# Performance work log

Hardware: AMD Instinct MI355X
Metric: run time of the kernel (lower is better)

Reference implementation:

```python
import jax, jax.numpy as jnp
import numpy as np

B, N, E, D, H, HW, L = 16, 32, 256, 256, 8, 784, 4
DH = D // H
FF = 4 * D
BN = B * N
BE = B * E
SCALE = 1.0 / np.sqrt(DH)


def _ln(x, g, b):
    m = x.mean(-1, keepdims=True)
    v = ((x - m) ** 2).mean(-1, keepdims=True)
    return (x - m) * jax.lax.rsqrt(v + 1e-5) * g + b


def setup_inputs() -> dict:
    key = jax.random.key(0)
    ks = iter(jax.random.split(key, 64))
    def w(shape, s=0.05):
        return jax.random.normal(next(ks), shape, jnp.float32) * s
    inp = {
        'nodes': w((B, N, D), 1.0),
        'edges': w((B, E, D), 1.0),
        'images': w((B, HW, D), 1.0),
        'mask': jnp.zeros((B * H, N + E, HW), jnp.float32),
        'node_enc': w((BN, D), 1.0),
        'edge_enc': w((BE, D), 1.0),
        'ln1_g': jnp.ones((L, D), jnp.float32), 'ln1_b': jnp.zeros((L, D), jnp.float32),
        'Wqkv': w((L, D, 3 * D)), 'bqkv': jnp.zeros((L, 3 * D), jnp.float32),
        'Wo': w((L, D, D)), 'bo': jnp.zeros((L, D), jnp.float32),
        'ls1': jnp.full((L, D), 0.1, jnp.float32),
        'ln2_g': jnp.ones((L, D), jnp.float32), 'ln2_b': jnp.zeros((L, D), jnp.float32),
        'Wn1': w((L, D, D)), 'bn1': jnp.zeros((L, D), jnp.float32),
        'Wn2': w((L, D, D)), 'bn2': jnp.zeros((L, D), jnp.float32),
        'We': w((L, D, D)), 'be': jnp.zeros((L, D), jnp.float32),
        'attn_p': w((L, H, DH), 1.0),
        'Weo': w((L, D, D)), 'beo': jnp.zeros((L, D), jnp.float32),
        'Wno': w((L, D, D)), 'bno': jnp.zeros((L, D), jnp.float32),
        'ls2': jnp.full((L, D), 0.1, jnp.float32),
        'ln3_g': jnp.ones((L, D), jnp.float32), 'ln3_b': jnp.zeros((L, D), jnp.float32),
        'W1': w((L, D, FF)), 'b1': jnp.zeros((L, FF), jnp.float32),
        'W2': w((L, FF, D)), 'b2': jnp.zeros((L, D), jnp.float32),
        'ls3': jnp.full((L, D), 0.1, jnp.float32),
        'edge_index': jax.random.randint(next(ks), (2, BE), 0, BN, jnp.int32),
    }
    return inp


def reference(nodes, edges, images, mask, node_enc, edge_enc,
              ln1_g, ln1_b, Wqkv, bqkv, Wo, bo, ls1,
              ln2_g, ln2_b, Wn1, bn1, Wn2, bn2, We, be, attn_p, Weo, beo, Wno, bno, ls2,
              ln3_g, ln3_b, W1, b1, W2, b2, ls3, edge_index):
    idx0, idx1 = edge_index[0], edge_index[1]
    ne = jnp.concatenate([nodes, edges], axis=1)  # [B, N+E, D]
    mask4 = mask.reshape(B, H, N + E, HW)
    for l in range(L):
        # cross-attention ne -> images
        ne1n = _ln(ne, ln1_g[l], ln1_b[l])
        q = (ne1n @ Wqkv[l, :, :D] + bqkv[l, :D]).reshape(B, N + E, H, DH)
        k = (images @ Wqkv[l, :, D:2 * D] + bqkv[l, D:2 * D]).reshape(B, HW, H, DH)
        v = (images @ Wqkv[l, :, 2 * D:] + bqkv[l, 2 * D:]).reshape(B, HW, H, DH)
        scores = jnp.einsum('bqhd,bkhd->bhqk', q, k) * SCALE + mask4
        attn = jax.nn.softmax(scores, axis=-1)
        ctx = jnp.einsum('bhqk,bkhd->bqhd', attn, v).reshape(B, N + E, D)
        ne1 = ne + ls1[l] * (ctx @ Wo[l] + bo[l])
        # modified GAT on flattened graph
        ne2n = _ln(ne1, ln2_g[l], ln2_b[l])
        nodes_f = ne2n[:, :N].reshape(BN, D) + node_enc
        edges_f = ne2n[:, N:].reshape(BE, D) + edge_enc
        fn = (nodes_f @ Wn1[l] + bn1[l])[idx0]
        sn = (nodes_f @ Wn2[l] + bn2[l])[idx0]  # NOTE: original code uses edge_index[0] here too
        ep = edges_f @ We[l] + be[l]
        hidden = jax.nn.gelu(fn + sn + ep, approximate=False)  # [BE, D]
        pres = (hidden.reshape(BE, H, DH) * attn_p[l]).sum(-1)  # [BE, H]
        mseg = jax.ops.segment_max(pres, idx0, num_segments=BN)
        expv = jnp.exp(pres - mseg[idx0])
        denom = jax.ops.segment_sum(expv, idx0, num_segments=BN)
        alpha = expv / denom[idx0]  # scatter_softmax over destination nodes
        new_edges = hidden @ Weo[l] + beo[l]
        vals = (nodes_f[idx1] + new_edges) @ Wno[l] + bno[l]
        vals = vals.reshape(BE, H, DH) * alpha[..., None]
        new_nodes = jax.ops.segment_sum(vals.reshape(BE, D), idx0, num_segments=BN)
        gat = jnp.concatenate([new_nodes.reshape(B, N, D), new_edges.reshape(B, E, D)], axis=1)
        ne2 = ne1 + ls2[l] * gat
        # FFN
        ne3n = _ln(ne2, ln3_g[l], ln3_b[l])
        ffn = jax.nn.gelu(ne3n @ W1[l] + b1[l], approximate=False) @ W2[l] + b2[l]
        ne = ne2 + ls3[l] * ffn
    return ne
```

## Files before the change

kernel.cpp:

```cpp
#include <hip/hip_runtime.h>
#include <math.h>

static constexpr int B_  = 16;
static constexpr int N_  = 32;
static constexpr int E_  = 256;
static constexpr int D_  = 256;
static constexpr int H_  = 8;
static constexpr int HW_ = 784;
static constexpr int L_  = 4;
static constexpr int DH_ = 32;
static constexpr int FF_ = 1024;
static constexpr int BN_ = 512;
static constexpr int BE_ = 4096;
static constexpr int NE_ = 288;
static constexpr int NC_ = 13;
static constexpr int NBLK_ = B_ * H_ * 9;
#define SCALE_ 0.17677669529663687f

static constexpr size_t LAYER_W = 1114112;
static constexpr size_t OFF_Q   = 0;
static constexpr size_t OFF_K   = 65536;
static constexpr size_t OFF_WO  = 196608;
static constexpr size_t OFF_WN1 = 262144;
static constexpr size_t OFF_WE  = 393216;
static constexpr size_t OFF_WEO = 458752;
static constexpr size_t OFF_WNO = 524288;
static constexpr size_t OFF_W1  = 589824;
static constexpr size_t OFF_W2  = 851968;

typedef __attribute__((ext_vector_type(8))) short bf16x8;
typedef __attribute__((ext_vector_type(4))) float f32x4;

typedef __attribute__((address_space(1))) const unsigned int gas_uint;
typedef __attribute__((address_space(3))) unsigned int las_uint;

__device__ __forceinline__ void gload16(const unsigned short* g, unsigned short* lds) {
    __builtin_amdgcn_global_load_lds((gas_uint*)g, (las_uint*)lds, 16, 0, 0);
}

__device__ __forceinline__ float gelu_f(float x) {
    return 0.5f * x * (1.0f + erff(x * 0.7071067811865476f));
}

__device__ __forceinline__ unsigned short f2bf(float x) {
    unsigned u = __float_as_uint(x);
    u += 0x7FFFu + ((u >> 16) & 1u);
    return (unsigned short)(u >> 16);
}
__device__ __forceinline__ unsigned pack2bf(float a, float b) {
    return (unsigned)f2bf(a) | ((unsigned)f2bf(b) << 16);
}
__device__ __forceinline__ float bf2f(unsigned short u) {
    return __uint_as_float(((unsigned)u) << 16);
}


__global__ void concat_kernel(const float* __restrict__ nodes, const float* __restrict__ edges,
                              float* __restrict__ ne) {
    int tid = blockIdx.x * 256 + threadIdx.x;
    int d = tid & 255;
    int row = tid >> 8;
    int b = row / NE_, pos = row % NE_;
    float v = (pos < N_) ? nodes[(size_t)(b * N_ + pos) * D_ + d]
                         : edges[(size_t)(b * E_ + (pos - N_)) * D_ + d];
    ne[tid] = v;
}

__global__ void imgcast_kernel(const float* __restrict__ img, unsigned short* __restrict__ out) {
    int tid = blockIdx.x * 256 + threadIdx.x;
    const float* p = img + (size_t)tid * 8;
    float4 a = *(const float4*)(p);
    float4 b = *(const float4*)(p + 4);
    uint4 o = make_uint4(pack2bf(a.x, a.y), pack2bf(a.z, a.w),
                         pack2bf(b.x, b.y), pack2bf(b.z, b.w));
    *(uint4*)&out[(size_t)tid * 8] = o;
}

__global__ void zeroinit_kernel(int* counts, int* maskflag) {
    int t = blockIdx.x * 256 + threadIdx.x;
    if (t < BN_) counts[t] = 0;
    if (t == 0) *maskflag = 0;
}

__global__ __launch_bounds__(256) void maskchk_kernel(const float* __restrict__ mask,
                                                      int* __restrict__ flag) {
    const size_t total = (size_t)B_ * H_ * NE_ * HW_ / 4;
    const uint4* m = (const uint4*)mask;
    unsigned acc = 0;
    for (size_t i = (size_t)blockIdx.x * 256 + threadIdx.x; i < total; i += (size_t)gridDim.x * 256) {
        uint4 v = m[i];
        acc |= v.x | v.y | v.z | v.w;
    }
    unsigned long long bal = __ballot(acc != 0);
    if (bal != 0 && (threadIdx.x & 63) == (__ffsll((long long)bal) - 1))
        atomicOr(flag, 1);
}

__global__ __launch_bounds__(128) void premask_kernel(const float* __restrict__ mask,
                                                      unsigned short* __restrict__ pmask,
                                                      const int* __restrict__ flag) {
    if (*flag == 0) return;
    const int bid = blockIdx.x;
    const int c = bid % NC_;
    const int bq = bid / NC_;
    const int h = bq & 7;
    const int qt = (bq >> 3) % 9;
    const int b = (bq >> 3) / 9;
    const int q0 = qt * 32, c0 = c * 64;
    __shared__ float ts[32][68];
    const int t = threadIdx.x;
    const int row = t >> 2, cg = (t & 3) * 16;
    const float* mrow = mask + ((size_t)(b * H_ + h) * NE_ + q0 + row) * (size_t)HW_;
    #pragma unroll
    for (int i = 0; i < 4; ++i) {
        int col = c0 + cg + i * 4;
        float4 m4;
        if (col + 4 <= HW_) {
            m4 = *(const float4*)(mrow + col);
        } else {
            m4.x = (col + 0 < HW_) ? mrow[col + 0] : -1e30f;
            m4.y = (col + 1 < HW_) ? mrow[col + 1] : -1e30f;
            m4.z = (col + 2 < HW_) ? mrow[col + 2] : -1e30f;
            m4.w = (col + 3 < HW_) ? mrow[col + 3] : -1e30f;
        }
        *(float4*)&ts[row][cg + i * 4] = m4;
    }
    __syncthreads();
    const int w = t >> 6, lg = (t & 63) >> 4, lr = t & 15;
    const int r0 = w * 16 + lg * 4;
    unsigned u[8];
    #pragma unroll
    for (int rg = 0; rg < 4; ++rg) {
        u[rg * 2 + 0] = pack2bf(ts[r0 + rg][0 * 16 + lr], ts[r0 + rg][1 * 16 + lr]);
        u[rg * 2 + 1] = pack2bf(ts[r0 + rg][2 * 16 + lr], ts[r0 + rg][3 * 16 + lr]);
    }
    uint4* dst = (uint4*)(pmask + (size_t)bid * 2048 + t * 16);
    dst[0] = make_uint4(u[0], u[1], u[2], u[3]);
    dst[1] = make_uint4(u[4], u[5], u[6], u[7]);
}

__device__ __forceinline__ float ln_from_val(float v, int d,
                                             const float* __restrict__ g, const float* __restrict__ bta,
                                             float* sh1, float* sh2) {
    float s = v, s2 = v * v;
    #pragma unroll
    for (int o = 32; o >= 1; o >>= 1) { s += __shfl_down(s, o); s2 += __shfl_down(s2, o); }
    int lane = d & 63, w = d >> 6;
    if (lane == 0) { sh1[w] = s; sh2[w] = s2; }
    __syncthreads();
    if (d == 0) {
        float a = sh1[0] + sh1[1] + sh1[2] + sh1[3];
        float c = sh2[0] + sh2[1] + sh2[2] + sh2[3];
        sh1[0] = a; sh2[0] = c;
    }
    __syncthreads();
    float mean = sh1[0] * (1.0f / D_);
    float var  = sh2[0] * (1.0f / D_) - mean * mean;
    float rstd = rsqrtf(var + 1e-5f);
    return (v - mean) * rstd * g[d] + bta[d];
}

__global__ __launch_bounds__(256) void ln_kernel(const float* __restrict__ x,
                                                 unsigned short* __restrict__ y,
                                                 const float* __restrict__ g,
                                                 const float* __restrict__ bta) {
    __shared__ float sh1[4], sh2[4];
    const int row = blockIdx.x, d = threadIdx.x;
    float v = x[(size_t)row * D_ + d];
    y[(size_t)row * D_ + d] = f2bf(ln_from_val(v, d, g, bta, sh1, sh2));
}

__global__ __launch_bounds__(256) void ln2enc_kernel(const float* __restrict__ x,
                                                     const float* __restrict__ g,
                                                     const float* __restrict__ bta,
                                                     const float* __restrict__ node_enc,
                                                     const float* __restrict__ edge_enc,
                                                     unsigned short* __restrict__ nodes_f,
                                                     unsigned short* __restrict__ edges_f) {
    __shared__ float sh1[4], sh2[4];
    const int row = blockIdx.x, d = threadIdx.x;
    float v = x[(size_t)row * D_ + d];
    float val = ln_from_val(v, d, g, bta, sh1, sh2);
    int b = row / NE_, pos = row % NE_;
    if (pos < N_) {
        int rn = b * N_ + pos;
        nodes_f[(size_t)rn * D_ + d] = f2bf(val + node_enc[(size_t)rn * D_ + d]);
    } else {
        int re = b * E_ + (pos - N_);
        edges_f[(size_t)re * D_ + d] = f2bf(val + edge_enc[(size_t)re * D_ + d]);
    }
}

__global__ __launch_bounds__(256) void gatres_ln_kernel(
    float* __restrict__ ne, const float* __restrict__ new_nodes,
    const float* __restrict__ new_edges, const float* __restrict__ ls2l,
    const float* __restrict__ g, const float* __restrict__ bta,
    unsigned short* __restrict__ lnb) {
    __shared__ float sh1[4], sh2[4];
    const int row = blockIdx.x, d = threadIdx.x;
    int b = row / NE_, pos = row % NE_;
    float gv = (pos < N_) ? new_nodes[(size_t)(b * N_ + pos) * D_ + d]
                          : new_edges[(size_t)(b * E_ + (pos - N_)) * D_ + d];
    float v = ne[(size_t)row * D_ + d] + ls2l[d] * gv;
    ne[(size_t)row * D_ + d] = v;
    lnb[(size_t)row * D_ + d] = f2bf(ln_from_val(v, d, g, bta, sh1, sh2));
}

__global__ __launch_bounds__(256) void wtrans_kernel(
    const float* __restrict__ Wqkv, const float* __restrict__ Wo,
    const float* __restrict__ Wn1,  const float* __restrict__ Wn2,
    const float* __restrict__ We,   const float* __restrict__ Weo,
    const float* __restrict__ Wno,  const float* __restrict__ W1,
    const float* __restrict__ W2,   unsigned short* __restrict__ wT)
{
    const int bid = blockIdx.x;
    const int l = bid / 1088;
    int tl = bid % 1088;
    const float* src; int ld, K, Nn; unsigned short* dst;
    if (tl < 576) {
        int mid = tl >> 6; tl &= 63;
        K = 256; Nn = 256;
        if (mid < 3) {
            src = Wqkv + (size_t)l * 256 * 768 + mid * 256; ld = 768;
            dst = wT + (size_t)l * LAYER_W + (size_t)mid * 65536;
        } else {
            const float* bases[6] = {Wo, Wn1, Wn2, We, Weo, Wno};
            src = bases[mid - 3] + (size_t)l * 65536; ld = 256;
            dst = wT + (size_t)l * LAYER_W + OFF_WO + (size_t)(mid - 3) * 65536;
        }
    } else if (tl < 832) {
        tl -= 576; K = 256; Nn = 1024;
        src = W1 + (size_t)l * 262144; ld = 1024;
        dst = wT + (size_t)l * LAYER_W + OFF_W1;
    } else {
        tl -= 832; K = 1024; Nn = 256;
        src = W2 + (size_t)l * 262144; ld = 256;
        dst = wT + (size_t)l * LAYER_W + OFF_W2;
    }
    const int ntn = Nn >> 5;
    const int k0 = (tl / ntn) << 5, n0 = (tl % ntn) << 5;
    __shared__ float ts[32][33];
    const int t = threadIdx.x;
    const int kl = t >> 5, nl = t & 31;
    #pragma unroll
    for (int rr = 0; rr < 4; ++rr)
        ts[kl + rr * 8][nl] = src[(size_t)(k0 + kl + rr * 8) * ld + n0 + nl];
    __syncthreads();
    const int onl = t >> 3, okl = (t & 7) << 2;
    ushort4 o;
    o.x = f2bf(ts[okl + 0][onl]); o.y = f2bf(ts[okl + 1][onl]);
    o.z = f2bf(ts[okl + 2][onl]); o.w = f2bf(ts[okl + 3][onl]);
    *(ushort4*)&dst[(size_t)(n0 + onl) * K + k0 + okl] = o;
}


struct GArgs {
    const unsigned short* A;
    const unsigned short* Bt;
    const float* bias;
    const float* bias2;
    void* C;
    int lda, ldc, K, outbf, nbx;
};

template<int MODE, int OUTBF>
__global__ __launch_bounds__(256) void mgemm_kernel(
    const unsigned short* __restrict__ A, int lda,
    const unsigned short* __restrict__ Bt,
    const float* __restrict__ bias,
    const float* __restrict__ bias2,
    const float* __restrict__ res,
    const float* __restrict__ ls,
    void* __restrict__ Cv, int ldc, int K)
{
    __shared__ __align__(16) unsigned short As[64 * 64];
    __shared__ __align__(16) unsigned short Bs[64 * 64];
    const int m0 = blockIdx.y * 64, n0 = blockIdx.x * 64;
    const int t = threadIdx.x;
    const int l = t & 63, w = t >> 6;
    const int wr = (w >> 1) * 32, wc = (w & 1) * 32;
    const int frow = l & 15, kg = l >> 4;
    const int srow = w * 8 + (l >> 3);
    const int scolh = 8 * ((l & 7) ^ (l >> 3));
    const int ldsoff = w * 512;
    const int sw = (frow & 7) << 3;
    f32x4 acc[2][2];
    acc[0][0] = (f32x4){0.f,0.f,0.f,0.f}; acc[0][1] = acc[0][0];
    acc[1][0] = acc[0][0];                acc[1][1] = acc[0][0];
    for (int k0 = 0; k0 < K; k0 += 64) {
        const unsigned short* ga = A  + (size_t)(m0 + srow) * lda + k0 + scolh;
        const unsigned short* gb = Bt + (size_t)(n0 + srow) * K   + k0 + scolh;
        gload16(ga,                As + ldsoff);
        gload16(ga + 32 * lda,     As + ldsoff + 2048);
        gload16(gb,                Bs + ldsoff);
        gload16(gb + (size_t)32 * K, Bs + ldsoff + 2048);
        __syncthreads();
        #pragma unroll
        for (int kk = 0; kk < 2; ++kk) {
            const int off = (kk * 32 + kg * 8) ^ sw;
            bf16x8 af0 = *(const bf16x8*)&As[(wr + frow) * 64 + off];
            bf16x8 af1 = *(const bf16x8*)&As[(wr + 16 + frow) * 64 + off];
            bf16x8 bf0 = *(const bf16x8*)&Bs[(wc + frow) * 64 + off];
            bf16x8 bf1 = *(const bf16x8*)&Bs[(wc + 16 + frow) * 64 + off];
            acc[0][0] = __builtin_amdgcn_mfma_f32_16x16x32_bf16(af0, bf0, acc[0][0], 0, 0, 0);
            acc[0][1] = __builtin_amdgcn_mfma_f32_16x16x32_bf16(af0, bf1, acc[0][1], 0, 0, 0);
            acc[1][0] = __builtin_amdgcn_mfma_f32_16x16x32_bf16(af1, bf0, acc[1][0], 0, 0, 0);
            acc[1][1] = __builtin_amdgcn_mfma_f32_16x16x32_bf16(af1, bf1, acc[1][1], 0, 0, 0);
        }
        __syncthreads();
    }
    #pragma unroll
    for (int fr = 0; fr < 2; ++fr) {
        #pragma unroll
        for (int fc = 0; fc < 2; ++fc) {
            int n = n0 + wc + fc * 16 + frow;
            float bv = (bias2 != nullptr && n >= 256) ? bias2[n - 256] : bias[n];
            float lv = (MODE == 2) ? ls[n] : 0.f;
            #pragma unroll
            for (int rg = 0; rg < 4; ++rg) {
                int m = m0 + wr + fr * 16 + kg * 4 + rg;
                float vv = acc[fr][fc][rg] + bv;
                if (MODE == 1) vv = gelu_f(vv);
                if (MODE == 2) vv = res[(size_t)m * ldc + n] + lv * vv;
                if (OUTBF) ((unsigned short*)Cv)[(size_t)m * ldc + n] = f2bf(vv);
                else       ((float*)Cv)[(size_t)m * ldc + n] = vv;
            }
        }
    }
}

__global__ __launch_bounds__(256) void mgemm2_kernel(GArgs g0, GArgs g1, int nblk0) {
    const bool first = (int)blockIdx.x < nblk0;
    GArgs g = first ? g0 : g1;
    const int bid = first ? blockIdx.x : blockIdx.x - nblk0;
    __shared__ __align__(16) unsigned short As[64 * 64];
    __shared__ __align__(16) unsigned short Bs[64 * 64];
    const int m0 = (bid / g.nbx) * 64, n0 = (bid % g.nbx) * 64;
    const int t = threadIdx.x;
    const int l = t & 63, w = t >> 6;
    const int wr = (w >> 1) * 32, wc = (w & 1) * 32;
    const int frow = l & 15, kg = l >> 4;
    const int srow = w * 8 + (l >> 3);
    const int scolh = 8 * ((l & 7) ^ (l >> 3));
    const int ldsoff = w * 512;
    const int sw = (frow & 7) << 3;
    f32x4 acc[2][2];
    acc[0][0] = (f32x4){0.f,0.f,0.f,0.f}; acc[0][1] = acc[0][0];
    acc[1][0] = acc[0][0];                acc[1][1] = acc[0][0];
    for (int k0 = 0; k0 < g.K; k0 += 64) {
        const unsigned short* ga = g.A  + (size_t)(m0 + srow) * g.lda + k0 + scolh;
        const unsigned short* gb = g.Bt + (size_t)(n0 + srow) * g.K   + k0 + scolh;
        gload16(ga,                  As + ldsoff);
        gload16(ga + 32 * g.lda,     As + ldsoff + 2048);
        gload16(gb,                  Bs + ldsoff);
        gload16(gb + (size_t)32 * g.K, Bs + ldsoff + 2048);
        __syncthreads();
        #pragma unroll
        for (int kk = 0; kk < 2; ++kk) {
            const int off = (kk * 32 + kg * 8) ^ sw;
            bf16x8 af0 = *(const bf16x8*)&As[(wr + frow) * 64 + off];
            bf16x8 af1 = *(const bf16x8*)&As[(wr + 16 + frow) * 64 + off];
            bf16x8 bf0 = *(const bf16x8*)&Bs[(wc + frow) * 64 + off];
            bf16x8 bf1 = *(const bf16x8*)&Bs[(wc + 16 + frow) * 64 + off];
            acc[0][0] = __builtin_amdgcn_mfma_f32_16x16x32_bf16(af0, bf0, acc[0][0], 0, 0, 0);
            acc[0][1] = __builtin_amdgcn_mfma_f32_16x16x32_bf16(af0, bf1, acc[0][1], 0, 0, 0);
            acc[1][0] = __builtin_amdgcn_mfma_f32_16x16x32_bf16(af1, bf0, acc[1][0], 0, 0, 0);
            acc[1][1] = __builtin_amdgcn_mfma_f32_16x16x32_bf16(af1, bf1, acc[1][1], 0, 0, 0);
        }
        __syncthreads();
    }
    #pragma unroll
    for (int fr = 0; fr < 2; ++fr) {
        #pragma unroll
        for (int fc = 0; fc < 2; ++fc) {
            int n = n0 + wc + fc * 16 + frow;
            float bv = (g.bias2 != nullptr && n >= 256) ? g.bias2[n - 256] : g.bias[n];
            #pragma unroll
            for (int rg = 0; rg < 4; ++rg) {
                int m = m0 + wr + fr * 16 + kg * 4 + rg;
                float vv = acc[fr][fc][rg] + bv;
                if (g.outbf) ((unsigned short*)g.C)[(size_t)m * g.ldc + n] = f2bf(vv);
                else         ((float*)g.C)[(size_t)m * g.ldc + n] = vv;
            }
        }
    }
}

__global__ __launch_bounds__(128) void attn_kernel(
    const unsigned short* __restrict__ q, const unsigned short* __restrict__ kv,
    const unsigned short* __restrict__ pmask, const int* __restrict__ maskflag,
    unsigned short* __restrict__ ctx)
{
    const int bid = blockIdx.x;
    const int h = bid & 7;
    const int qt = (bid >> 3) % 9;
    const int b = (bid >> 3) / 9;
    const int q0 = qt * 32;
    const int t = threadIdx.x;
    const int w = t >> 6, l = t & 63;
    const int lr = l & 15, lg = l >> 4;
    const int hasmask = *maskflag;

    __shared__ unsigned short Ks[2][64][40];
    __shared__ unsigned short Vs[2][32][72];
    __shared__ unsigned short Pl[2][16][72];

    bf16x8 qfrag = *(const bf16x8*)(q + ((size_t)(b * NE_ + q0 + w * 16 + lr)) * D_ + h * DH_ + lg * 8);

    const int kkey = t >> 1, kdh = (t & 1) * 16;
    const int vdh = (t & 7) * 4, vk0 = (t >> 3) * 2;
    const unsigned short* kbase = kv + ((size_t)b * HW_) * 512 + h * DH_;
    const unsigned short* vbase = kv + ((size_t)b * HW_) * 512 + 256 + h * DH_;
    const uint4* mbase = (const uint4*)(pmask + (size_t)bid * NC_ * 2048 + t * 16);

    uint4 kq0, kq1;
    ushort4 va[2], vb4[2];
    uint4 mc0 = make_uint4(0,0,0,0), mc1 = mc0, mn0 = mc0, mn1 = mc0;

    auto issue_kv = [&](int c0) {
        {
            int key = c0 + kkey;
            bool ok = key < HW_;
            const unsigned short* kp = kbase + (size_t)(ok ? key : 0) * 512 + kdh;
            kq0 = *(const uint4*)(kp);
            kq1 = *(const uint4*)(kp + 8);
            if (!ok) { kq0 = make_uint4(0,0,0,0); kq1 = kq0; }
        }
        #pragma unroll
        for (int r = 0; r < 2; ++r) {
            int key = c0 + vk0 + 32 * r;
            bool ok0 = key < HW_, ok1 = (key + 1) < HW_;
            const unsigned short* vp = vbase + (size_t)(ok0 ? key : 0) * 512 + vdh;
            va[r]  = *(const ushort4*)(vp);
            vb4[r] = *(const ushort4*)(vp + (ok1 ? 512 : 0));
            if (!ok0) va[r]  = make_ushort4(0,0,0,0);
            if (!ok1) vb4[r] = make_ushort4(0,0,0,0);
        }
    };
    auto write_kv = [&](int bufi) {
        *(uint4*)&Ks[bufi][kkey][kdh]     = kq0;
        *(uint4*)&Ks[bufi][kkey][kdh + 8] = kq1;
        #pragma unroll
        for (int r = 0; r < 2; ++r) {
            const unsigned short* a = (const unsigned short*)&va[r];
            const unsigned short* c = (const unsigned short*)&vb4[r];
            #pragma unroll
            for (int i = 0; i < 4; ++i)
                *(unsigned*)&Vs[bufi][vdh + i][vk0 + 32 * r] = (unsigned)a[i] | ((unsigned)c[i] << 16);
        }
    };

    f32x4 oacc[2];
    oacc[0] = (f32x4){0.f, 0.f, 0.f, 0.f}; oacc[1] = oacc[0];
    float m_i[4] = {-INFINITY, -INFINITY, -INFINITY, -INFINITY};
    float l_i[4] = {0.f, 0.f, 0.f, 0.f};

    issue_kv(0);
    if (hasmask) { mc0 = mbase[0]; mc1 = mbase[1]; }
    write_kv(0);
    if (hasmask) { mn0 = mbase[128]; mn1 = mbase[129]; }
    __syncthreads();

    for (int c = 0; c < NC_; ++c) {
        const int c0 = c * 64;
        const int cb = c & 1, nb = cb ^ 1;
        if (c + 1 < NC_) issue_kv(c0 + 64);

        f32x4 sacc[4];
        #pragma unroll
        for (int fc = 0; fc < 4; ++fc) {
            sacc[fc] = (f32x4){0.f, 0.f, 0.f, 0.f};
            bf16x8 kf = *(const bf16x8*)&Ks[cb][fc * 16 + lr][lg * 8];
            sacc[fc] = __builtin_amdgcn_mfma_f32_16x16x32_bf16(qfrag, kf, sacc[fc], 0, 0, 0);
        }
        float s[4][4];
        if (hasmask) {
            unsigned uw[8] = {mc0.x, mc0.y, mc0.z, mc0.w, mc1.x, mc1.y, mc1.z, mc1.w};
            #pragma unroll
            for (int rg = 0; rg < 4; ++rg) {
                s[0][rg] = sacc[0][rg] * SCALE_ + bf2f((unsigned short)(uw[rg * 2] & 0xffff));
                s[1][rg] = sacc[1][rg] * SCALE_ + bf2f((unsigned short)(uw[rg * 2] >> 16));
                s[2][rg] = sacc[2][rg] * SCALE_ + bf2f((unsigned short)(uw[rg * 2 + 1] & 0xffff));
                s[3][rg] = sacc[3][rg] * SCALE_ + bf2f((unsigned short)(uw[rg * 2 + 1] >> 16));
            }
        } else {
            const bool tailc = (c == NC_ - 1);
            #pragma unroll
            for (int fc = 0; fc < 4; ++fc) {
                float pad = (tailc && (c0 + fc * 16 + lr) >= HW_) ? -1e30f : 0.f;
                #pragma unroll
                for (int rg = 0; rg < 4; ++rg)
                    s[fc][rg] = sacc[fc][rg] * SCALE_ + pad;
            }
        }

        float mloc[4];
        #pragma unroll
        for (int rg = 0; rg < 4; ++rg)
            mloc[rg] = fmaxf(fmaxf(s[0][rg], s[1][rg]), fmaxf(s[2][rg], s[3][rg]));
        #pragma unroll
        for (int off = 1; off < 16; off <<= 1)
            #pragma unroll
            for (int rg = 0; rg < 4; ++rg)
                mloc[rg] = fmaxf(mloc[rg], __shfl_xor(mloc[rg], off));
        float scl[4], lloc[4];
        #pragma unroll
        for (int rg = 0; rg < 4; ++rg) {
            float mn = fmaxf(m_i[rg], mloc[rg]);
            scl[rg] = __expf(m_i[rg] - mn);
            m_i[rg] = mn;
        }
        #pragma unroll
        for (int rg = 0; rg < 4; ++rg) {
            float acc = 0.f;
            #pragma unroll
            for (int fc = 0; fc < 4; ++fc) {
                float p = __expf(s[fc][rg] - m_i[rg]);
                s[fc][rg] = p;
                acc += p;
            }
            lloc[rg] = acc;
        }
        #pragma unroll
        for (int off = 1; off < 16; off <<= 1)
            #pragma unroll
            for (int rg = 0; rg < 4; ++rg)
                lloc[rg] += __shfl_xor(lloc[rg], off);
        #pragma unroll
        for (int rg = 0; rg < 4; ++rg) {
            l_i[rg] = l_i[rg] * scl[rg] + lloc[rg];
            oacc[0][rg] *= scl[rg];
            oacc[1][rg] *= scl[rg];
        }

        #pragma unroll
        for (int fc = 0; fc < 4; ++fc)
            #pragma unroll
            for (int rg = 0; rg < 4; ++rg)
                Pl[w][lg * 4 + rg][fc * 16 + lr] = f2bf(s[fc][rg]);
        #pragma unroll
        for (int ks2 = 0; ks2 < 2; ++ks2) {
            bf16x8 pf = *(const bf16x8*)&Pl[w][lr][ks2 * 32 + lg * 8];
            #pragma unroll
            for (int d2 = 0; d2 < 2; ++d2) {
                bf16x8 vf = *(const bf16x8*)&Vs[cb][d2 * 16 + lr][ks2 * 32 + lg * 8];
                oacc[d2] = __builtin_amdgcn_mfma_f32_16x16x32_bf16(pf, vf, oacc[d2], 0, 0, 0);
            }
        }

        if (hasmask) {
            mc0 = mn0; mc1 = mn1;
            if (c + 2 < NC_) {
                mn0 = mbase[(c + 2) * 128];
                mn1 = mbase[(c + 2) * 128 + 1];
            }
        }
        if (c + 1 < NC_) {
            write_kv(nb);
            __syncthreads();
        }
    }

    unsigned short* cbase = ctx + ((size_t)(b * NE_ + q0 + w * 16 + lg * 4)) * D_ + h * DH_;
    #pragma unroll
    for (int rg = 0; rg < 4; ++rg) {
        float inv = 1.0f / l_i[rg];
        #pragma unroll
        for (int d2 = 0; d2 < 2; ++d2)
            cbase[(size_t)rg * D_ + d2 * 16 + lr] = f2bf(oacc[d2][rg] * inv);
    }
}


__global__ __launch_bounds__(256) void hidden_kernel(
    const float* __restrict__ gn12,
    unsigned short* __restrict__ hid, const int* __restrict__ idx0,
    const float* __restrict__ attn_p_l, float* __restrict__ pres) {
    int e = blockIdx.x;
    int d = threadIdx.x;
    int n = idx0[e];
    float x = bf2f(hid[(size_t)e * D_ + d]) + gn12[(size_t)n * 512 + d] + gn12[(size_t)n * 512 + 256 + d];
    float hv = gelu_f(x);
    hid[(size_t)e * D_ + d] = f2bf(hv);
    float pr = hv * attn_p_l[d];
    #pragma unroll
    for (int o = 1; o < 32; o <<= 1) pr += __shfl_xor(pr, o);
    if ((d & 31) == 0) pres[e * H_ + (d >> 5)] = pr;
}

__global__ void segsoft_kernel(const float* __restrict__ pres, const int* __restrict__ csr_off,
                               const int* __restrict__ csr_perm,
                               float* __restrict__ mseg, float* __restrict__ denom) {
    int tid = blockIdx.x * 256 + threadIdx.x;
    int n = tid >> 3, h = tid & 7;
    int s = csr_off[n], e2 = csr_off[n + 1];
    float mx = -INFINITY;
    for (int i = s; i < e2; ++i) mx = fmaxf(mx, pres[csr_perm[i] * H_ + h]);
    float sum = 0.f;
    for (int i = s; i < e2; ++i) sum += expf(pres[csr_perm[i] * H_ + h] - mx);
    mseg[tid] = mx;
    denom[tid] = sum;
}

__global__ void vin_kernel(const unsigned short* __restrict__ nodes_f,
                           const float* __restrict__ new_edges,
                           const int* __restrict__ idx1, unsigned short* __restrict__ vin) {
    int tid = blockIdx.x * 256 + threadIdx.x;
    int e = tid >> 8, d = tid & 255;
    vin[tid] = f2bf(bf2f(nodes_f[(size_t)idx1[e] * D_ + d]) + new_edges[tid]);
}

__global__ __launch_bounds__(256) void nodeagg_kernel(
    const float* __restrict__ vals, const float* __restrict__ pres,
    const float* __restrict__ mseg, const float* __restrict__ denom,
    const int* __restrict__ csr_off, const int* __restrict__ csr_perm,
    float* __restrict__ new_nodes) {
    int n = blockIdx.x;
    int d = threadIdx.x;
    int s = csr_off[n], e2 = csr_off[n + 1];
    int h = d >> 5;
    float ms = mseg[n * H_ + h];
    float rd = 1.0f / denom[n * H_ + h];
    float acc = 0.f;
    for (int i = s; i < e2; ++i) {
        int e = csr_perm[i];
        float a = expf(pres[e * H_ + h] - ms) * rd;
        acc += vals[(size_t)e * D_ + d] * a;
    }
    new_nodes[(size_t)n * D_ + d] = acc;
}


__global__ void csr_count(const int* __restrict__ idx0, int* __restrict__ counts) {
    int e = blockIdx.x * 256 + threadIdx.x;
    if (e < BE_) atomicAdd(&counts[idx0[e]], 1);
}

__global__ __launch_bounds__(512) void csr_scan(const int* __restrict__ counts, int* __restrict__ csr_off) {
    __shared__ int buf[BN_];
    int t = threadIdx.x;
    int c = counts[t];
    buf[t] = c;
    __syncthreads();
    for (int o = 1; o < BN_; o <<= 1) {
        int add = (t >= o) ? buf[t - o] : 0;
        __syncthreads();
        buf[t] += add;
        __syncthreads();
    }
    csr_off[t] = buf[t] - c;
    if (t == BN_ - 1) csr_off[BN_] = buf[t];
}

__global__ __launch_bounds__(64) void csr_fill(const int* __restrict__ idx0,
                                               const int* __restrict__ csr_off,
                                               int* __restrict__ csr_perm) {
    int n = blockIdx.x;
    int lane = threadIdx.x;
    int w = csr_off[n];
    for (int c0 = 0; c0 < BE_; c0 += 64) {
        int e = c0 + lane;
        bool m = (idx0[e] == n);
        unsigned long long bal = __ballot(m);
        if (m) {
            int pre = __popcll(bal & ((1ull << lane) - 1ull));
            csr_perm[w + pre] = e;
        }
        w += __popcll(bal);
    }
}


static void launch_mgemm(hipStream_t s, int mode, int outbf,
                         const unsigned short* A, int lda, const unsigned short* Bt,
                         const float* bias, const float* bias2, const float* res, const float* ls,
                         void* C, int ldc, int M, int N, int K) {
    dim3 g(N / 64, M / 64);
    if (mode == 0) {
        if (outbf) mgemm_kernel<0,1><<<g, 256, 0, s>>>(A, lda, Bt, bias, bias2, res, ls, C, ldc, K);
        else       mgemm_kernel<0,0><<<g, 256, 0, s>>>(A, lda, Bt, bias, bias2, res, ls, C, ldc, K);
    } else if (mode == 1) {
        mgemm_kernel<1,1><<<g, 256, 0, s>>>(A, lda, Bt, bias, bias2, res, ls, C, ldc, K);
    } else {
        mgemm_kernel<2,0><<<g, 256, 0, s>>>(A, lda, Bt, bias, bias2, res, ls, C, ldc, K);
    }
}

extern "C" void kernel_launch(void* const* d_in, const int* in_sizes, int n_in,
                              void* d_out, int out_size, void* d_ws, size_t ws_size,
                              hipStream_t stream) {
    const float* nodes    = (const float*)d_in[0];
    const float* edges    = (const float*)d_in[1];
    const float* images   = (const float*)d_in[2];
    const float* mask     = (const float*)d_in[3];
    const float* node_enc = (const float*)d_in[4];
    const float* edge_enc = (const float*)d_in[5];
    const float* ln1_g = (const float*)d_in[6];
    const float* ln1_b = (const float*)d_in[7];
    const float* Wqkv  = (const float*)d_in[8];
    const float* bqkv  = (const float*)d_in[9];
    const float* Wo    = (const float*)d_in[10];
    const float* bo    = (const float*)d_in[11];
    const float* ls1   = (const float*)d_in[12];
    const float* ln2_g = (const float*)d_in[13];
    const float* ln2_b = (const float*)d_in[14];
    const float* Wn1   = (const float*)d_in[15];
    const float* bn1   = (const float*)d_in[16];
    const float* Wn2   = (const float*)d_in[17];
    const float* bn2   = (const float*)d_in[18];
    const float* We    = (const float*)d_in[19];
    const float* be    = (const float*)d_in[20];
    const float* attn_p= (const float*)d_in[21];
    const float* Weo   = (const float*)d_in[22];
    const float* beo   = (const float*)d_in[23];
    const float* Wno   = (const float*)d_in[24];
    const float* bno   = (const float*)d_in[25];
    const float* ls2   = (const float*)d_in[26];
    const float* ln3_g = (const float*)d_in[27];
    const float* ln3_b = (const float*)d_in[28];
    const float* W1    = (const float*)d_in[29];
    const float* b1    = (const float*)d_in[30];
    const float* W2    = (const float*)d_in[31];
    const float* b2    = (const float*)d_in[32];
    const float* ls3   = (const float*)d_in[33];
    const int*   edge_index = (const int*)d_in[34];
    const int* idx0 = edge_index;
    const int* idx1 = edge_index + BE_;

    float* ne = (float*)d_out;

    float* cur = (float*)d_ws;
    auto alloc = [&](size_t nfl) { float* p = cur; cur += nfl; return p; };
    auto allocbf = [&](size_t nbf) { float* p = cur; cur += (nbf + 1) / 2; return (unsigned short*)p; };

    unsigned short* lnbuf   = allocbf((size_t)B_ * NE_ * D_);
    unsigned short* qb      = allocbf((size_t)B_ * NE_ * D_);
    unsigned short* kvb     = allocbf((size_t)B_ * HW_ * 512);
    unsigned short* ffnh    = kvb;
    unsigned short* imgbf   = allocbf((size_t)B_ * HW_ * D_);
    unsigned short* ctxb    = allocbf((size_t)B_ * NE_ * D_);
    unsigned short* nodes_f = allocbf((size_t)BN_ * D_);
    unsigned short* edges_f = allocbf((size_t)BE_ * D_);
    unsigned short* hid     = allocbf((size_t)BE_ * D_);
    unsigned short* vin     = allocbf((size_t)BE_ * D_);
    unsigned short* pmaskb  = allocbf((size_t)NBLK_ * NC_ * 2048);
    float* gn12     = alloc((size_t)BN_ * 512);
    float* pres     = alloc((size_t)BE_ * H_);
    float* mseg     = alloc((size_t)BN_ * H_);
    float* denom    = alloc((size_t)BN_ * H_);
    float* new_edges= alloc((size_t)BE_ * D_);
    float* valsb    = alloc((size_t)BE_ * D_);
    float* new_nodes= alloc((size_t)BN_ * D_);
    int* counts   = (int*)cur; cur += BN_;
    int* csr_off  = (int*)cur; cur += BN_ + 4;
    int* csr_perm = (int*)cur; cur += BE_;
    int* maskflag = (int*)cur; cur += 4;
    cur = (float*)(((uintptr_t)cur + 255) & ~(uintptr_t)255);
    unsigned short* wT = (unsigned short*)cur;

    zeroinit_kernel<<<2, 256, 0, stream>>>(counts, maskflag);
    maskchk_kernel<<<2048, 256, 0, stream>>>(mask, maskflag);
    wtrans_kernel<<<4 * 1088, 256, 0, stream>>>(Wqkv, Wo, Wn1, Wn2, We, Weo, Wno, W1, W2, wT);
    imgcast_kernel<<<(B_ * HW_ * D_) / (256 * 8), 256, 0, stream>>>(images, imgbf);
    premask_kernel<<<NBLK_ * NC_, 128, 0, stream>>>(mask, pmaskb, maskflag);
    csr_count<<<BE_ / 256, 256, 0, stream>>>(idx0, counts);
    csr_scan<<<1, 512, 0, stream>>>(counts, csr_off);
    csr_fill<<<BN_, 64, 0, stream>>>(idx0, csr_off, csr_perm);
    concat_kernel<<<(B_ * NE_ * D_) / 256, 256, 0, stream>>>(nodes, edges, ne);

    for (int l = 0; l < L_; ++l) {
        const unsigned short* wTl = wT + (size_t)l * LAYER_W;
        const float* bqkv_l = bqkv + (size_t)l * 3 * D_;

        ln_kernel<<<B_ * NE_, 256, 0, stream>>>(ne, lnbuf, ln1_g + l * D_, ln1_b + l * D_);
        {
            GArgs gq { lnbuf, wTl + OFF_Q, bqkv_l, nullptr, qb, 256, 256, 256, 1, 4 };
            GArgs gkv{ imgbf, wTl + OFF_K, bqkv_l + D_, nullptr, kvb, 256, 512, 256, 1, 8 };
            int nb0 = (B_ * NE_ / 64) * 4;
            int nb1 = (B_ * HW_ / 64) * 8;
            mgemm2_kernel<<<nb0 + nb1, 256, 0, stream>>>(gq, gkv, nb0);
        }
        attn_kernel<<<NBLK_, 128, 0, stream>>>(qb, kvb, pmaskb, maskflag, ctxb);
        launch_mgemm(stream, 2, 0, ctxb, D_, wTl + OFF_WO, bo + l * D_, nullptr, ne, ls1 + l * D_,
                     ne, D_, B_ * NE_, D_, D_);

        ln2enc_kernel<<<B_ * NE_, 256, 0, stream>>>(ne, ln2_g + l * D_, ln2_b + l * D_,
                                                    node_enc, edge_enc, nodes_f, edges_f);
        {
            GArgs gn { nodes_f, wTl + OFF_WN1, bn1 + l * D_, bn2 + l * D_, gn12, 256, 512, 256, 0, 8 };
            GArgs ge { edges_f, wTl + OFF_WE,  be + l * D_,  nullptr,      hid,  256, 256, 256, 1, 4 };
            int nb0 = (BN_ / 64) * 8;
            int nb1 = (BE_ / 64) * 4;
            mgemm2_kernel<<<nb0 + nb1, 256, 0, stream>>>(gn, ge, nb0);
        }
        hidden_kernel<<<BE_, 256, 0, stream>>>(gn12, hid, idx0, attn_p + (size_t)l * H_ * DH_, pres);
        segsoft_kernel<<<(BN_ * H_) / 256, 256, 0, stream>>>(pres, csr_off, csr_perm, mseg, denom);
        launch_mgemm(stream, 0, 0, hid, D_, wTl + OFF_WEO, beo + l * D_, nullptr, nullptr, nullptr,
                     new_edges, D_, BE_, D_, D_);
        vin_kernel<<<(BE_ * D_) / 256, 256, 0, stream>>>(nodes_f, new_edges, idx1, vin);
        launch_mgemm(stream, 0, 0, vin, D_, wTl + OFF_WNO, bno + l * D_, nullptr, nullptr, nullptr,
                     valsb, D_, BE_, D_, D_);
        nodeagg_kernel<<<BN_, 256, 0, stream>>>(valsb, pres, mseg, denom, csr_off, csr_perm, new_nodes);
        gatres_ln_kernel<<<B_ * NE_, 256, 0, stream>>>(ne, new_nodes, new_edges, ls2 + l * D_,
                                                       ln3_g + l * D_, ln3_b + l * D_, lnbuf);

        launch_mgemm(stream, 1, 1, lnbuf, D_, wTl + OFF_W1, b1 + l * FF_, nullptr, nullptr, nullptr,
                     ffnh, FF_, B_ * NE_, FF_, D_);
        launch_mgemm(stream, 2, 0, ffnh, FF_, wTl + OFF_W2, b2 + l * D_, nullptr, ne, ls3 + l * D_,
                     ne, D_, B_ * NE_, D_, FF_);
    }
}
```

Baseline: 619.6 us.

## Hoist K/V projections for all layers into one batched 128-tile GEMM

The image K/V projection depends only on the images and the weights, so all four layers' K/V projections are computed once before the layer loop. This is a single 12544x2048x256 GEMM using a new 128x128-tile MFMA kernel that writes into a wide buffer, and the attention kernel reads each layer's slice with a 2048-element stride. The FFN W1 GEMM also moves to the 128-tile kernel with fused GELU. The cost is a larger workspace (a separate ffnh buffer and a 4x wider KV buffer), and attention reads K/V rows with a larger stride.

After: 649.9 us. 1.05x slower.

```diff
diff --git a/kernel.cpp b/kernel.cpp
--- a/kernel.cpp
+++ b/kernel.cpp
@@ -19,7 +19,6 @@
 
 static constexpr size_t LAYER_W = 1114112;
 static constexpr size_t OFF_Q   = 0;
-static constexpr size_t OFF_K   = 65536;
 static constexpr size_t OFF_WO  = 196608;
 static constexpr size_t OFF_WN1 = 262144;
 static constexpr size_t OFF_WE  = 393216;
@@ -211,7 +210,8 @@
     const float* __restrict__ Wn1,  const float* __restrict__ Wn2,
     const float* __restrict__ We,   const float* __restrict__ Weo,
     const float* __restrict__ Wno,  const float* __restrict__ W1,
-    const float* __restrict__ W2,   unsigned short* __restrict__ wT)
+    const float* __restrict__ W2,   unsigned short* __restrict__ wT,
+    unsigned short* __restrict__ kvwT)
 {
     const int bid = blockIdx.x;
     const int l = bid / 1088;
@@ -220,9 +220,12 @@
     if (tl < 576) {
         int mid = tl >> 6; tl &= 63;
         K = 256; Nn = 256;
-        if (mid < 3) {
+        if (mid == 0) {
+            src = Wqkv + (size_t)l * 256 * 768; ld = 768;
+            dst = wT + (size_t)l * LAYER_W + OFF_Q;
+        } else if (mid < 3) {
             src = Wqkv + (size_t)l * 256 * 768 + mid * 256; ld = 768;
-            dst = wT + (size_t)l * LAYER_W + (size_t)mid * 65536;
+            dst = kvwT + ((size_t)l * 512 + (size_t)(mid - 1) * 256) * 256;
         } else {
             const float* bases[6] = {Wo, Wn1, Wn2, We, Weo, Wno};
             src = bases[mid - 3] + (size_t)l * 65536; ld = 256;
@@ -386,6 +389,73 @@
     }
 }
 
+template<int MODE>
+__global__ __launch_bounds__(256) void mgemm128_kernel(
+    const unsigned short* __restrict__ A, int lda,
+    const unsigned short* __restrict__ Bt,
+    const float* __restrict__ bias,
+    unsigned short* __restrict__ C, int ldc, int K, int nbx)
+{
+    __shared__ __align__(16) unsigned short As[128 * 64];
+    __shared__ __align__(16) unsigned short Bs[128 * 64];
+    const int bid = blockIdx.x;
+    const int m0 = (bid / nbx) * 128, n0 = (bid % nbx) * 128;
+    const int t = threadIdx.x;
+    const int l = t & 63, w = t >> 6;
+    const int wr = (w >> 1) * 64, wc = (w & 1) * 64;
+    const int frow = l & 15, kg = l >> 4;
+    const int srow = w * 8 + (l >> 3);
+    const int scolh = 8 * ((l & 7) ^ (l >> 3));
+    const int ldsoff = w * 512;
+    const int sw = (frow & 7) << 3;
+    f32x4 acc[4][4];
+    #pragma unroll
+    for (int i = 0; i < 4; ++i)
+        #pragma unroll
+        for (int j = 0; j < 4; ++j) acc[i][j] = (f32x4){0.f, 0.f, 0.f, 0.f};
+    for (int k0 = 0; k0 < K; k0 += 64) {
+        #pragma unroll
+        for (int j = 0; j < 4; ++j) {
+            gload16(A  + (size_t)(m0 + j * 32 + srow) * lda + k0 + scolh, As + j * 2048 + ldsoff);
+            gload16(Bt + (size_t)(n0 + j * 32 + srow) * K   + k0 + scolh, Bs + j * 2048 + ldsoff);
+        }
+        __syncthreads();
+        #pragma unroll
+        for (int kk = 0; kk < 2; ++kk) {
+            const int off = (kk * 32 + kg * 8) ^ sw;
+            bf16x8 af[4], bf[4];
+            #pragma unroll
+            for (int i = 0; i < 4; ++i) {
+                af[i] = *(const bf16x8*)&As[(wr + i * 16 + frow) * 64 + off];
+                bf[i] = *(const bf16x8*)&Bs[(wc + i * 16 + frow) * 64 + off];
+            }
+            #pragma unroll
+            for (int i = 0; i < 4; ++i)
+                #pragma unroll
+                for (int j = 0; j < 4; ++j)
+                    acc[i][j] = __builtin_amdgcn_mfma_f32_16x16x32_bf16(af[i], bf[j], acc[i][j], 0, 0, 0);
+        }
+        __syncthreads();
+    }
+    #pragma unroll
+    for (int fr = 0; fr < 4; ++fr) {
+        #pragma unroll
+        for (int fc = 0; fc < 4; ++fc) {
+            int n = n0 + wc + fc * 16 + frow;
+            float bv;
+            if (MODE == 3) bv = bias[(n >> 9) * 768 + 256 + (n & 511)];
+            else           bv = bias[n];
+            #pragma unroll
+            for (int rg = 0; rg < 4; ++rg) {
+                int m = m0 + wr + fr * 16 + kg * 4 + rg;
+                float vv = acc[fr][fc][rg] + bv;
+                if (MODE == 1) vv = gelu_f(vv);
+                C[(size_t)m * ldc + n] = f2bf(vv);
+            }
+        }
+    }
+}
+
 __global__ __launch_bounds__(128) void attn_kernel(
     const unsigned short* __restrict__ q, const unsigned short* __restrict__ kv,
     const unsigned short* __restrict__ pmask, const int* __restrict__ maskflag,
@@ -409,8 +479,8 @@
 
     const int kkey = t >> 1, kdh = (t & 1) * 16;
     const int vdh = (t & 7) * 4, vk0 = (t >> 3) * 2;
-    const unsigned short* kbase = kv + ((size_t)b * HW_) * 512 + h * DH_;
-    const unsigned short* vbase = kv + ((size_t)b * HW_) * 512 + 256 + h * DH_;
+    const unsigned short* kbase = kv + ((size_t)b * HW_) * 2048 + h * DH_;
+    const unsigned short* vbase = kbase + 256;
     const uint4* mbase = (const uint4*)(pmask + (size_t)bid * NC_ * 2048 + t * 16);
 
     uint4 kq0, kq1;
@@ -421,7 +491,7 @@
         {
             int key = c0 + kkey;
             bool ok = key < HW_;
-            const unsigned short* kp = kbase + (size_t)(ok ? key : 0) * 512 + kdh;
+            const unsigned short* kp = kbase + (size_t)(ok ? key : 0) * 2048 + kdh;
             kq0 = *(const uint4*)(kp);
             kq1 = *(const uint4*)(kp + 8);
             if (!ok) { kq0 = make_uint4(0,0,0,0); kq1 = kq0; }
@@ -430,9 +500,9 @@
         for (int r = 0; r < 2; ++r) {
             int key = c0 + vk0 + 32 * r;
             bool ok0 = key < HW_, ok1 = (key + 1) < HW_;
-            const unsigned short* vp = vbase + (size_t)(ok0 ? key : 0) * 512 + vdh;
+            const unsigned short* vp = vbase + (size_t)(ok0 ? key : 0) * 2048 + vdh;
             va[r]  = *(const ushort4*)(vp);
-            vb4[r] = *(const ushort4*)(vp + (ok1 ? 512 : 0));
+            vb4[r] = *(const ushort4*)(vp + (ok1 ? 2048 : 0));
             if (!ok0) va[r]  = make_ushort4(0,0,0,0);
             if (!ok1) vb4[r] = make_ushort4(0,0,0,0);
         }
@@ -735,8 +805,8 @@
 
     unsigned short* lnbuf   = allocbf((size_t)B_ * NE_ * D_);
     unsigned short* qb      = allocbf((size_t)B_ * NE_ * D_);
-    unsigned short* kvb     = allocbf((size_t)B_ * HW_ * 512);
-    unsigned short* ffnh    = kvb;
+    unsigned short* kvall   = allocbf((size_t)B_ * HW_ * 2048);
+    unsigned short* ffnh    = allocbf((size_t)B_ * NE_ * FF_);
     unsigned short* imgbf   = allocbf((size_t)B_ * HW_ * D_);
     unsigned short* ctxb    = allocbf((size_t)B_ * NE_ * D_);
     unsigned short* nodes_f = allocbf((size_t)BN_ * D_);
@@ -744,6 +814,7 @@
     unsigned short* hid     = allocbf((size_t)BE_ * D_);
     unsigned short* vin     = allocbf((size_t)BE_ * D_);
     unsigned short* pmaskb  = allocbf((size_t)NBLK_ * NC_ * 2048);
+    unsigned short* kvwT    = allocbf((size_t)L_ * 512 * 256);
     float* gn12     = alloc((size_t)BN_ * 512);
     float* pres     = alloc((size_t)BE_ * H_);
     float* mseg     = alloc((size_t)BN_ * H_);
@@ -760,27 +831,24 @@
 
     zeroinit_kernel<<<2, 256, 0, stream>>>(counts, maskflag);
     maskchk_kernel<<<2048, 256, 0, stream>>>(mask, maskflag);
-    wtrans_kernel<<<4 * 1088, 256, 0, stream>>>(Wqkv, Wo, Wn1, Wn2, We, Weo, Wno, W1, W2, wT);
+    wtrans_kernel<<<4 * 1088, 256, 0, stream>>>(Wqkv, Wo, Wn1, Wn2, We, Weo, Wno, W1, W2, wT, kvwT);
     imgcast_kernel<<<(B_ * HW_ * D_) / (256 * 8), 256, 0, stream>>>(images, imgbf);
     premask_kernel<<<NBLK_ * NC_, 128, 0, stream>>>(mask, pmaskb, maskflag);
     csr_count<<<BE_ / 256, 256, 0, stream>>>(idx0, counts);
     csr_scan<<<1, 512, 0, stream>>>(counts, csr_off);
     csr_fill<<<BN_, 64, 0, stream>>>(idx0, csr_off, csr_perm);
     concat_kernel<<<(B_ * NE_ * D_) / 256, 256, 0, stream>>>(nodes, edges, ne);
+    mgemm128_kernel<3><<<(B_ * HW_ / 128) * (2048 / 128), 256, 0, stream>>>(
+        imgbf, 256, kvwT, bqkv, kvall, 2048, 256, 2048 / 128);
 
     for (int l = 0; l < L_; ++l) {
         const unsigned short* wTl = wT + (size_t)l * LAYER_W;
         const float* bqkv_l = bqkv + (size_t)l * 3 * D_;
 
         ln_kernel<<<B_ * NE_, 256, 0, stream>>>(ne, lnbuf, ln1_g + l * D_, ln1_b + l * D_);
-        {
-            GArgs gq { lnbuf, wTl + OFF_Q, bqkv_l, nullptr, qb, 256, 256, 256, 1, 4 };
-            GArgs gkv{ imgbf, wTl + OFF_K, bqkv_l + D_, nullptr, kvb, 256, 512, 256, 1, 8 };
-            int nb0 = (B_ * NE_ / 64) * 4;
-            int nb1 = (B_ * HW_ / 64) * 8;
-            mgemm2_kernel<<<nb0 + nb1, 256, 0, stream>>>(gq, gkv, nb0);
-        }
-        attn_kernel<<<NBLK_, 128, 0, stream>>>(qb, kvb, pmaskb, maskflag, ctxb);
+        launch_mgemm(stream, 0, 1, lnbuf, D_, wTl + OFF_Q, bqkv_l, nullptr, nullptr, nullptr,
+                     qb, D_, B_ * NE_, D_, D_);
+        attn_kernel<<<NBLK_, 128, 0, stream>>>(qb, kvall + (size_t)l * 512, pmaskb, maskflag, ctxb);
         launch_mgemm(stream, 2, 0, ctxb, D_, wTl + OFF_WO, bo + l * D_, nullptr, ne, ls1 + l * D_,
                      ne, D_, B_ * NE_, D_, D_);
 
@@ -804,8 +872,8 @@
         gatres_ln_kernel<<<B_ * NE_, 256, 0, stream>>>(ne, new_nodes, new_edges, ls2 + l * D_,
                                                        ln3_g + l * D_, ln3_b + l * D_, lnbuf);
 
-        launch_mgemm(stream, 1, 1, lnbuf, D_, wTl + OFF_W1, b1 + l * FF_, nullptr, nullptr, nullptr,
-                     ffnh, FF_, B_ * NE_, FF_, D_);
+        mgemm128_kernel<1><<<(B_ * NE_ / 128) * (FF_ / 128), 256, 0, stream>>>(
+            lnbuf, 256, wTl + OFF_W1, b1 + l * FF_, ffnh, FF_, 256, FF_ / 128);
         launch_mgemm(stream, 2, 0, ffnh, FF_, wTl + OFF_W2, b2 + l * D_, nullptr, ne, ls3 + l * D_,
                      ne, D_, B_ * NE_, D_, FF_);
     }
```
